# Kernel tuning notes

Hardware: AMD Instinct MI355X
Metric: run time of the kernel (lower is better)

The kernel has to match this reference:

```python
import jax, jax.numpy as jnp
import numpy as np
from jax import lax

NUM_POINTS = 2048  # M, from init_kwargs


def setup_inputs() -> dict:
    key = jax.random.key(0)
    points = jax.random.normal(key, (16, 65536, 3), dtype=jnp.float32)
    return {"points": points}


def farthest_point_sampling(points, num_samples):
    """Iterative D-FPS. points: (B, N, 3) -> indices (B, M) int32."""
    B, N, _ = points.shape
    BIG = jnp.asarray(1e10, points.dtype)

    def step(carry, _):
        min_dist, last_idx = carry          # (B, N), (B,)
        last_pt = jnp.take_along_axis(points, last_idx[:, None, None], axis=1)  # (B,1,3)
        d = jnp.sum((points - last_pt) ** 2, axis=-1)  # (B, N) squared dist to newest centroid
        min_dist = jnp.minimum(min_dist, d)
        nxt = jnp.argmax(min_dist, axis=1).astype(jnp.int32)  # farthest remaining point
        return (min_dist, nxt), nxt

    first = jnp.zeros((B,), dtype=jnp.int32)  # seed with point 0 (standard FPS convention)
    init = (jnp.full((B, N), BIG, points.dtype), first)
    _, rest = lax.scan(step, init, None, length=num_samples - 1)  # (M-1, B)
    indices = jnp.concatenate([first[None, :], rest], axis=0)      # (M, B)
    return indices.T                                                # (B, M)


def reference(points):
    B, N, _ = points.shape
    if N <= NUM_POINTS:
        idx = jnp.broadcast_to(jnp.arange(N, dtype=jnp.int32)[None, :], (B, N))
        return idx
    return farthest_point_sampling(points, NUM_POINTS)
```

## Files before the change

kernel.cpp:

```cpp
#include <hip/hip_runtime.h>


#define N_PTS   65536
#define M_SAMP  2048
#define NT      512
#define BPB     16
#define PTS_BLK (N_PTS / BPB)
#define PPT     (PTS_BLK / NT)
#define NWAVES  (NT / 64)
#define NBATCH  16
#define SLOT_U64 16

typedef unsigned long long u64;

__device__ __forceinline__ u64 ld_agent(const u64* a) {
  return __hip_atomic_load(a, __ATOMIC_RELAXED, __HIP_MEMORY_SCOPE_AGENT);
}
__device__ __forceinline__ void st_agent(u64* a, u64 v) {
  __hip_atomic_store(a, v, __ATOMIC_RELAXED, __HIP_MEMORY_SCOPE_AGENT);
}

__global__ __launch_bounds__(NT, 2)
void fps_multi(const float* __restrict__ pts, int* __restrict__ out,
               u64* __restrict__ ws) {
  const int rank = blockIdx.x;
  const int b    = blockIdx.y;
  const float* __restrict__ p = pts + (size_t)b * (size_t)(N_PTS * 3);
  int* __restrict__ o = out + (size_t)b * M_SAMP;
  const int t = threadIdx.x;
  const int base = rank * PTS_BLK;

  __shared__ float  s_pts[PTS_BLK * 3];
  __shared__ double s_bv[NWAVES];
  __shared__ int    s_bi[NWAVES];
  __shared__ float  s_c[3];

  for (int i = t; i < PTS_BLK * 3; i += NT)
    s_pts[i] = p[base * 3 + i];
  if (rank == 0 && t == 0) o[0] = 0;
  if (t == 0) { s_c[0] = p[0]; s_c[1] = p[1]; s_c[2] = p[2]; }
  __syncthreads();

  double pd[PPT][3];
  double md[PPT];
#pragma unroll
  for (int j = 0; j < PPT; ++j) {
    const int l = t + j * NT;
    pd[j][0] = (double)s_pts[3 * l + 0];
    pd[j][1] = (double)s_pts[3 * l + 1];
    pd[j][2] = (double)s_pts[3 * l + 2];
    md[j] = 1e10;
  }

  for (int m = 1; m < M_SAMP; ++m) {
    const double cx = (double)s_c[0];
    const double cy = (double)s_c[1];
    const double cz = (double)s_c[2];

    double bestv = -1.0;
    int    besti = 0;

#pragma unroll
    for (int j = 0; j < PPT; ++j) {
      const double dx = __dsub_rn(pd[j][0], cx);
      const double dy = __dsub_rn(pd[j][1], cy);
      const double dz = __dsub_rn(pd[j][2], cz);
      const double d  = __dadd_rn(__dadd_rn(__dmul_rn(dx, dx),
                                            __dmul_rn(dy, dy)),
                                  __dmul_rn(dz, dz));
      const double nmd = fmin(md[j], d);
      md[j] = nmd;
      if (nmd > bestv) { bestv = nmd; besti = base + t + j * NT; }
    }

#pragma unroll
    for (int off = 32; off >= 1; off >>= 1) {
      const double ov = __shfl_xor(bestv, off, 64);
      const int    oi = __shfl_xor(besti, off, 64);
      if (ov > bestv || (ov == bestv && oi < besti)) { bestv = ov; besti = oi; }
    }
    if ((t & 63) == 0) { s_bv[t >> 6] = bestv; s_bi[t >> 6] = besti; }
    __syncthreads();

    if (t < 64) {
      if (t < NWAVES) {
        bestv = s_bv[t]; besti = s_bi[t];
#pragma unroll
        for (int off = NWAVES / 2; off >= 1; off >>= 1) {
          const double ov = __shfl_xor(bestv, off, 64);
          const int    oi = __shfl_xor(besti, off, 64);
          if (ov > bestv || (ov == bestv && oi < besti)) { bestv = ov; besti = oi; }
        }
      }
      const u64 mm  = (u64)(unsigned)m;
      const u64 grp = (u64)(((m & 1) * NBATCH + b) * BPB);
      if (t == 0) {
        u64* slot = ws + (grp + rank) * SLOT_U64;
        const int l = besti - base;
        const unsigned xb = __float_as_uint(s_pts[3 * l + 0]);
        const unsigned yb = __float_as_uint(s_pts[3 * l + 1]);
        const unsigned zb = __float_as_uint(s_pts[3 * l + 2]);
        const u64 vb = (u64)__double_as_longlong(bestv);
        const u64 ti = (mm << 16) | (u64)(unsigned)besti;
        st_agent(&slot[0], (vb << 32) | ti);
        st_agent(&slot[1], (vb & 0xFFFFFFFF00000000ull) | ti);
        st_agent(&slot[2], ((u64)xb << 32) | (mm << 16) | (u64)(yb >> 16));
        st_agent(&slot[3], ((u64)(yb & 0xFFFFu) << 48) | ((u64)zb << 16) | mm);
      }
      if (t < BPB) {
        const u64* rs = ws + (grp + t) * SLOT_U64;
        u64 A, B, C, D;
        for (;;) {
          A = ld_agent(rs + 0);
          B = ld_agent(rs + 1);
          C = ld_agent(rs + 2);
          D = ld_agent(rs + 3);
          const bool ok = (((A >> 16) & 0xFFFFull) == mm) &
                          (((B >> 16) & 0xFFFFull) == mm) &
                          (((C >> 16) & 0xFFFFull) == mm) &
                          ((D & 0xFFFFull) == mm);
          if (ok) break;
        }
        double v = __longlong_as_double(
            (long long)((B & 0xFFFFFFFF00000000ull) | (A >> 32)));
        int   i = (int)(A & 0xFFFFull);
        float fx = __uint_as_float((unsigned)(C >> 32));
        float fy = __uint_as_float((unsigned)(((C & 0xFFFFull) << 16) | (D >> 48)));
        float fz = __uint_as_float((unsigned)((D >> 16) & 0xFFFFFFFFull));
        int r = t;
#pragma unroll
        for (int off = BPB / 2; off >= 1; off >>= 1) {
          const double ov = __shfl_xor(v, off, 64);
          const int    oi = __shfl_xor(i, off, 64);
          const int    orr = __shfl_xor(r, off, 64);
          if (ov > v || (ov == v && oi < i)) { v = ov; i = oi; r = orr; }
        }
        fx = __shfl(fx, r, 64);
        fy = __shfl(fy, r, 64);
        fz = __shfl(fz, r, 64);
        if (t == 0) {
          s_c[0] = fx; s_c[1] = fy; s_c[2] = fz;
          if (rank == 0) o[m] = i;
        }
      }
    }
    __syncthreads();
  }
}

extern "C" void kernel_launch(void* const* d_in, const int* in_sizes, int n_in,
                              void* d_out, int out_size, void* d_ws, size_t ws_size,
                              hipStream_t stream) {
  const float* pts = (const float*)d_in[0];
  int* out = (int*)d_out;
  const int B = in_sizes[0] / (N_PTS * 3);
  hipLaunchKernelGGL(fps_multi, dim3(BPB, B), dim3(NT), 0, stream,
                     pts, out, (u64*)d_ws);
}
```

Before: 5.839 ms.

## Add XCD-local fast path for inter-block exchange with 1D grid remap

Launches a 1D grid and remaps block ids so that the 16 blocks cooperating on a batch are likely to land on the same XCD under round-robin dispatch. Each block also publishes its candidate to a second slot with workgroup-scope stores, and readers poll that slot after an L1 invalidate. The idea is to cut the latency of the per-iteration cross-block barrier by keeping the exchange in the shared L2 of one XCD, falling back to agent-scope polling if the probe fails. Outputs are buffered in LDS and written once at the end. The approach relies on undocumented dispatch placement and cache behaviour, and it risks extra spin cost whenever the fast path misses.

```diff
diff --git a/kernel.cpp b/kernel.cpp
--- a/kernel.cpp
+++ b/kernel.cpp
@@ -9,7 +9,10 @@
 #define PPT     (PTS_BLK / NT)
 #define NWAVES  (NT / 64)
 #define NBATCH  16
-#define SLOT_U64 16
+#define SLOT_U64 8
+#define FAST_OFF (2 * NBATCH * BPB * SLOT_U64)
+#define PROBE_SPINS 64
+#define FAST_SPINS  64
 
 typedef unsigned long long u64;
 
@@ -18,13 +21,35 @@
 }
 __device__ __forceinline__ void st_agent(u64* a, u64 v) {
   __hip_atomic_store(a, v, __ATOMIC_RELAXED, __HIP_MEMORY_SCOPE_AGENT);
+}
+__device__ __forceinline__ u64 ld_wg(const u64* a) {
+  return __hip_atomic_load(a, __ATOMIC_RELAXED, __HIP_MEMORY_SCOPE_WORKGROUP);
+}
+__device__ __forceinline__ void st_wg(u64* a, u64 v) {
+  __hip_atomic_store(a, v, __ATOMIC_RELAXED, __HIP_MEMORY_SCOPE_WORKGROUP);
+}
+__device__ __forceinline__ void l1_inv() {
+  asm volatile("buffer_inv sc0" ::: "memory");
+}
+__device__ __forceinline__ bool tagok(u64 A, u64 B, u64 C, u64 D, u64 mm) {
+  return (((A >> 16) & 0xFFFFull) == mm) &
+         (((B >> 16) & 0xFFFFull) == mm) &
+         (((C >> 16) & 0xFFFFull) == mm) &
+         ((D & 0xFFFFull) == mm);
 }
 
 __global__ __launch_bounds__(NT, 2)
 void fps_multi(const float* __restrict__ pts, int* __restrict__ out,
                u64* __restrict__ ws) {
-  const int rank = blockIdx.x;
-  const int b    = blockIdx.y;
+  int b, rank;
+  if (gridDim.y == 1) {
+    const int lid  = blockIdx.x;
+    const int slot = lid >> 3;
+    b    = (lid & 7) + ((slot & 1) << 3);
+    rank = slot >> 1;
+  } else {
+    rank = blockIdx.x; b = blockIdx.y;
+  }
   const float* __restrict__ p = pts + (size_t)b * (size_t)(N_PTS * 3);
   int* __restrict__ o = out + (size_t)b * M_SAMP;
   const int t = threadIdx.x;
@@ -34,10 +59,11 @@
   __shared__ double s_bv[NWAVES];
   __shared__ int    s_bi[NWAVES];
   __shared__ float  s_c[3];
+  __shared__ int    s_out[M_SAMP];
 
   for (int i = t; i < PTS_BLK * 3; i += NT)
     s_pts[i] = p[base * 3 + i];
-  if (rank == 0 && t == 0) o[0] = 0;
+  if (t == 0) { s_out[0] = 0; }
   if (t == 0) { s_c[0] = p[0]; s_c[1] = p[1]; s_c[2] = p[2]; }
   __syncthreads();
 
@@ -51,6 +77,8 @@
     pd[j][2] = (double)s_pts[3 * l + 2];
     md[j] = 1e10;
   }
+
+  bool fast = false;
 
   for (int m = 1; m < M_SAMP; ++m) {
     const double cx = (double)s_c[0];
@@ -95,31 +123,63 @@
       const u64 mm  = (u64)(unsigned)m;
       const u64 grp = (u64)(((m & 1) * NBATCH + b) * BPB);
       if (t == 0) {
-        u64* slot = ws + (grp + rank) * SLOT_U64;
         const int l = besti - base;
         const unsigned xb = __float_as_uint(s_pts[3 * l + 0]);
         const unsigned yb = __float_as_uint(s_pts[3 * l + 1]);
         const unsigned zb = __float_as_uint(s_pts[3 * l + 2]);
         const u64 vb = (u64)__double_as_longlong(bestv);
         const u64 ti = (mm << 16) | (u64)(unsigned)besti;
-        st_agent(&slot[0], (vb << 32) | ti);
-        st_agent(&slot[1], (vb & 0xFFFFFFFF00000000ull) | ti);
-        st_agent(&slot[2], ((u64)xb << 32) | (mm << 16) | (u64)(yb >> 16));
-        st_agent(&slot[3], ((u64)(yb & 0xFFFFu) << 48) | ((u64)zb << 16) | mm);
+        const u64 Aw = (vb << 32) | ti;
+        const u64 Bw = (vb & 0xFFFFFFFF00000000ull) | ti;
+        const u64 Cw = ((u64)xb << 32) | (mm << 16) | (u64)(yb >> 16);
+        const u64 Dw = ((u64)(yb & 0xFFFFu) << 48) | ((u64)zb << 16) | mm;
+        u64* fsw = ws + FAST_OFF + (grp + rank) * SLOT_U64;
+        st_wg(fsw + 0, Aw);
+        st_wg(fsw + 1, Bw);
+        st_wg(fsw + 2, Cw);
+        st_wg(fsw + 3, Dw);
+        u64* s = ws + (grp + rank) * SLOT_U64;
+        st_agent(&s[0], Aw);
+        st_agent(&s[1], Bw);
+        st_agent(&s[2], Cw);
+        st_agent(&s[3], Dw);
       }
       if (t < BPB) {
-        const u64* rs = ws + (grp + t) * SLOT_U64;
         u64 A, B, C, D;
-        for (;;) {
-          A = ld_agent(rs + 0);
-          B = ld_agent(rs + 1);
-          C = ld_agent(rs + 2);
-          D = ld_agent(rs + 3);
-          const bool ok = (((A >> 16) & 0xFFFFull) == mm) &
-                          (((B >> 16) & 0xFFFFull) == mm) &
-                          (((C >> 16) & 0xFFFFull) == mm) &
-                          ((D & 0xFFFFull) == mm);
-          if (ok) break;
+        bool got = false;
+        const u64* fs = ws + FAST_OFF + (grp + t) * SLOT_U64;
+        if (fast) {
+          for (int sp = 0; sp < FAST_SPINS; ++sp) {
+            l1_inv();
+            A = ld_wg(fs + 0); B = ld_wg(fs + 1);
+            C = ld_wg(fs + 2); D = ld_wg(fs + 3);
+            if (tagok(A, B, C, D, mm)) { got = true; break; }
+            __builtin_amdgcn_s_sleep(1);
+          }
+          if (!got) fast = false;
+        }
+        if (!got) {
+          const u64* rs = ws + (grp + t) * SLOT_U64;
+          for (;;) {
+            A = ld_agent(rs + 0);
+            B = ld_agent(rs + 1);
+            C = ld_agent(rs + 2);
+            D = ld_agent(rs + 3);
+            if (tagok(A, B, C, D, mm)) break;
+          }
+          if (m == 1) {
+            u64 w0 = ld_wg(fs + 0), w1 = ld_wg(fs + 1);
+            u64 w2 = ld_wg(fs + 2), w3 = ld_wg(fs + 3);
+            asm volatile("" :: "v"(w0), "v"(w1), "v"(w2), "v"(w3));
+          } else if (m == 2) {
+            for (int sp = 0; sp < PROBE_SPINS && !fast; ++sp) {
+              l1_inv();
+              const u64 a2 = ld_wg(fs + 0), b2 = ld_wg(fs + 1);
+              const u64 c2 = ld_wg(fs + 2), d2 = ld_wg(fs + 3);
+              fast = tagok(a2, b2, c2, d2, mm);
+              if (!fast) __builtin_amdgcn_s_sleep(1);
+            }
+          }
         }
         double v = __longlong_as_double(
             (long long)((B & 0xFFFFFFFF00000000ull) | (A >> 32)));
@@ -140,12 +200,15 @@
         fz = __shfl(fz, r, 64);
         if (t == 0) {
           s_c[0] = fx; s_c[1] = fy; s_c[2] = fz;
-          if (rank == 0) o[m] = i;
+          if (rank == 0) s_out[m] = i;
         }
       }
     }
     __syncthreads();
   }
+
+  if (rank == 0)
+    for (int i = t; i < M_SAMP; i += NT) o[i] = s_out[i];
 }
 
 extern "C" void kernel_launch(void* const* d_in, const int* in_sizes, int n_in,
@@ -154,6 +217,11 @@
   const float* pts = (const float*)d_in[0];
   int* out = (int*)d_out;
   const int B = in_sizes[0] / (N_PTS * 3);
-  hipLaunchKernelGGL(fps_multi, dim3(BPB, B), dim3(NT), 0, stream,
-                     pts, out, (u64*)d_ws);
-}
+  if (B == NBATCH) {
+    hipLaunchKernelGGL(fps_multi, dim3(BPB * NBATCH), dim3(NT), 0, stream,
+                       pts, out, (u64*)d_ws);
+  } else {
+    hipLaunchKernelGGL(fps_multi, dim3(BPB, B), dim3(NT), 0, stream,
+                       pts, out, (u64*)d_ws);
+  }
+}
```

New measurement: 5.625 ms. 3.7% less time.
